# Optimization experiments

Hardware: AMD Instinct MI355X
Metric: run time of the kernel (lower is better)

## Reference

```python
import jax, jax.numpy as jnp
import numpy as np

HIDDEN = 2048
VOCAB = 50257


def setup_inputs() -> dict:
    key = jax.random.key(0)
    ks = jax.random.split(key, 9)
    s = 1.0 / np.sqrt(HIDDEN)
    return {
        "input": jax.random.randint(ks[0], (1,), 0, VOCAB, dtype=jnp.int64) if jax.config.jax_enable_x64 else jax.random.randint(ks[0], (1,), 0, VOCAB, dtype=jnp.int32),
        "hidden": jax.random.normal(ks[1], (1, 1, HIDDEN), dtype=jnp.float32),
        "embedding": jax.random.normal(ks[2], (VOCAB, HIDDEN), dtype=jnp.float32),
        "w_ih": jax.random.uniform(ks[3], (3 * HIDDEN, HIDDEN), jnp.float32, -s, s),
        "w_hh": jax.random.uniform(ks[4], (3 * HIDDEN, HIDDEN), jnp.float32, -s, s),
        "b_ih": jax.random.uniform(ks[5], (3 * HIDDEN,), jnp.float32, -s, s),
        "b_hh": jax.random.uniform(ks[6], (3 * HIDDEN,), jnp.float32, -s, s),
        "out_w": jax.random.uniform(ks[7], (VOCAB, HIDDEN), jnp.float32, -s, s),
        "out_b": jax.random.uniform(ks[8], (VOCAB,), jnp.float32, -s, s),
    }


def reference(input, hidden, embedding, w_ih, w_hh, b_ih, b_hh, out_w, out_b):
    # embedding lookup + view(1,1,-1) + relu  -> x: [H]
    x = jax.nn.relu(embedding[input[0]])
    h = hidden[0, 0]  # [H]
    # PyTorch GRU single step: gates ordered (r, z, n)
    gi = w_ih @ x + b_ih  # [3H]
    gh = w_hh @ h + b_hh  # [3H]
    i_r, i_z, i_n = jnp.split(gi, 3)
    h_r, h_z, h_n = jnp.split(gh, 3)
    r = jax.nn.sigmoid(i_r + h_r)
    z = jax.nn.sigmoid(i_z + h_z)
    n = jnp.tanh(i_n + r * h_n)
    h_new = (1.0 - z) * n + z * h  # [H]
    # output projection (nn.Linear: x @ W.T + b) + log_softmax(dim=1)
    logits = out_w @ h_new + out_b  # [V]
    logp = jax.nn.log_softmax(logits)[None, :]  # [1, V]
    return logp, h_new[None, None, :]
```

## Files before the change

kernel.cpp:

```cpp
#include <hip/hip_runtime.h>
#include <math.h>

#define H 2048
#define V 50257
#define NTHR 256
#define LB 512
#define NW (LB * 4)
#define ROWS_BASE 24
#define TAIL (V - ROWS_BASE * NW)

typedef unsigned long long u64;

#if defined(__has_builtin)
#if __has_builtin(__builtin_amdgcn_global_load_lds)
#define HAS_GLL 1
#endif
#endif
#ifndef HAS_GLL
#define HAS_GLL 0
#endif

__device__ __forceinline__ float wave_reduce_sum(float v) {
#pragma unroll
    for (int off = 32; off > 0; off >>= 1)
        v += __shfl_down(v, off, 64);
    return v;
}

__device__ __forceinline__ void online_comb(float& m, float& s, float om, float os) {
    float M = fmaxf(m, om);
    s = s * __expf(m - M) + os * __expf(om - M);
    m = M;
}

#if HAS_GLL
__device__ __forceinline__ void gl2lds16(const void* g, void* l) {
    __builtin_amdgcn_global_load_lds(
        (const __attribute__((address_space(1))) void*)g,
        (__attribute__((address_space(3))) void*)l, 16, 0, 0);
}
#endif

__global__ __launch_bounds__(384) void k_gru(
    const int* __restrict__ idx_p, const float* __restrict__ emb,
    const float* __restrict__ hid,
    const float* __restrict__ w_ih, const float* __restrict__ w_hh,
    const float* __restrict__ b_ih, const float* __restrict__ b_hh,
    float* __restrict__ hnew_ws, float* __restrict__ hnew_out,
    u64* __restrict__ partials) {
    __shared__ float xs[H];
    __shared__ float hs[H];
    __shared__ float partial[6][2];
    int tid = threadIdx.x;

    if (tid == 0 && blockIdx.x < LB) partials[blockIdx.x] = 0ull;

    long idx = (long)idx_p[0];
    const float4* embrow = (const float4*)(emb + idx * (long)H);
    for (int i = tid; i < H / 4; i += 384) {
        float4 e = embrow[i];
        e.x = fmaxf(e.x, 0.f); e.y = fmaxf(e.y, 0.f);
        e.z = fmaxf(e.z, 0.f); e.w = fmaxf(e.w, 0.f);
        ((float4*)xs)[i] = e;
        ((float4*)hs)[i] = ((const float4*)hid)[i];
    }
    __syncthreads();

    int wid = tid >> 6, lane = tid & 63;
    int gate = wid % 3;
    const float* W   = (wid < 3) ? w_ih : w_hh;
    const float* vec = (wid < 3) ? xs : hs;
    int j0 = blockIdx.x, j1 = blockIdx.x + 1024;
    const float4* r0 = (const float4*)(W + ((size_t)gate * H + j0) * (size_t)H);
    const float4* r1 = (const float4*)(W + ((size_t)gate * H + j1) * (size_t)H);

    float4 vreg[8];
#pragma unroll
    for (int it = 0; it < 8; ++it)
        vreg[it] = ((const float4*)vec)[it * 64 + lane];

    float a0 = 0.f, a1 = 0.f;
#pragma unroll
    for (int it = 0; it < 8; ++it) {
        float4 wa = r0[it * 64 + lane];
        float4 wb = r1[it * 64 + lane];
        a0 += wa.x * vreg[it].x + wa.y * vreg[it].y + wa.z * vreg[it].z + wa.w * vreg[it].w;
        a1 += wb.x * vreg[it].x + wb.y * vreg[it].y + wb.z * vreg[it].z + wb.w * vreg[it].w;
    }
    a0 = wave_reduce_sum(a0);
    a1 = wave_reduce_sum(a1);
    if (lane == 0) { partial[wid][0] = a0; partial[wid][1] = a1; }
    __syncthreads();

    if (tid < 2) {
        int j = (tid == 0) ? j0 : j1;
        float i_r = partial[0][tid] + b_ih[j];
        float i_z = partial[1][tid] + b_ih[H + j];
        float i_n = partial[2][tid] + b_ih[2 * H + j];
        float h_r = partial[3][tid] + b_hh[j];
        float h_z = partial[4][tid] + b_hh[H + j];
        float h_n = partial[5][tid] + b_hh[2 * H + j];
        float r = 1.f / (1.f + expf(-(i_r + h_r)));
        float z = 1.f / (1.f + expf(-(i_z + h_z)));
        float n = tanhf(i_n + r * h_n);
        float hv = (1.f - z) * n + z * hs[j];
        hnew_ws[j] = hv;
        hnew_out[j] = hv;
    }
}

__global__ __launch_bounds__(NTHR, 2) void k_logits_fused(
    const float* __restrict__ out_w, const float* __restrict__ out_b,
    const float* __restrict__ hnew, float* __restrict__ out,
    u64* __restrict__ partials) {
    __shared__ float hsm[H];
    __shared__ float stage[4][2][H];
    __shared__ float l_lds[4][25];
    __shared__ float pm[4], ps[4];
    __shared__ float c_s;
    const int tid = threadIdx.x, wid = tid >> 6, lane = tid & 63;
    const int gw = blockIdx.x * 4 + wid;
    const int nrows = ROWS_BASE + (gw < TAIL ? 1 : 0);

    for (int i = tid; i < H / 4; i += NTHR)
        ((float4*)hsm)[i] = ((const float4*)hnew)[i];
    float bias = 0.f;
    if (lane < nrows) {
        int r = (lane < ROWS_BASE) ? (gw + lane * NW) : (ROWS_BASE * NW + gw);
        bias = out_b[r];
    }
    asm volatile("" :: "v"(bias));
    __syncthreads();

    float4 vreg[8];
#pragma unroll
    for (int it = 0; it < 8; ++it)
        vreg[it] = ((const float4*)hsm)[it * 64 + lane];

    float* slot0 = &stage[wid][0][0];
    float* slot1 = &stage[wid][1][0];

    float m = -INFINITY, s = 0.f;

#if HAS_GLL
    auto issue_row = [&](int k) {
        int r = (k < ROWS_BASE) ? (gw + k * NW) : (ROWS_BASE * NW + gw);
        const char* gb = (const char*)(out_w + (size_t)r * H) + lane * 16;
        char* lb = (char*)((k & 1) ? slot1 : slot0);
#pragma unroll
        for (int c = 0; c < 8; ++c)
            gl2lds16(gb + c * 1024, lb + c * 1024);
    };

    issue_row(0);
    issue_row(1);
#pragma unroll 1
    for (int k = 0; k < nrows; ++k) {
        if (k == nrows - 1) {
            asm volatile("s_waitcnt vmcnt(0)" ::: "memory");
        } else {
            asm volatile("s_waitcnt vmcnt(8)" ::: "memory");
        }
        __builtin_amdgcn_sched_barrier(0);
        const float4* s4 = (const float4*)((k & 1) ? slot1 : slot0);
        float acc = 0.f;
#pragma unroll
        for (int it = 0; it < 8; ++it) {
            float4 w4 = s4[it * 64 + lane];
            acc += w4.x * vreg[it].x + w4.y * vreg[it].y + w4.z * vreg[it].z + w4.w * vreg[it].w;
        }
        acc = wave_reduce_sum(acc);
        float bk = __shfl(bias, k, 64);
        if (lane == 0) {
            float l = acc + bk;
            l_lds[wid][k] = l;
            online_comb(m, s, l, 1.0f);
        }
        if (k + 2 < nrows) issue_row(k + 2);
    }
#else
#pragma unroll 1
    for (int k = 0; k < nrows; ++k) {
        int r = (k < ROWS_BASE) ? (gw + k * NW) : (ROWS_BASE * NW + gw);
        const float4* row = (const float4*)(out_w + (size_t)r * H);
        float acc = 0.f;
#pragma unroll
        for (int it = 0; it < 8; ++it) {
            float4 w4 = row[it * 64 + lane];
            acc += w4.x * vreg[it].x + w4.y * vreg[it].y + w4.z * vreg[it].z + w4.w * vreg[it].w;
        }
        acc = wave_reduce_sum(acc);
        float bk = __shfl(bias, k, 64);
        if (lane == 0) {
            float l = acc + bk;
            l_lds[wid][k] = l;
            online_comb(m, s, l, 1.0f);
        }
    }
#endif

    if (lane == 0) { pm[wid] = m; ps[wid] = s; }
    __syncthreads();

    if (tid == 0) {
        float M = pm[0], S = ps[0];
        online_comb(M, S, pm[1], ps[1]);
        online_comb(M, S, pm[2], ps[2]);
        online_comb(M, S, pm[3], ps[3]);
        u64 pk = ((u64)__float_as_uint(S) << 32) | (u64)__float_as_uint(M);
        __hip_atomic_store(&partials[blockIdx.x], pk, __ATOMIC_RELAXED,
                           __HIP_MEMORY_SCOPE_AGENT);
    }
    __syncthreads();

    float mm = -INFINITY, ss = 0.f;
    for (int i = tid; i < LB; i += NTHR) {
        u64 pk;
        while ((pk = __hip_atomic_load(&partials[i], __ATOMIC_RELAXED,
                                       __HIP_MEMORY_SCOPE_AGENT)) == 0ull)
            __builtin_amdgcn_s_sleep(8);
        float pmv = __uint_as_float((unsigned)(pk & 0xffffffffu));
        float psv = __uint_as_float((unsigned)(pk >> 32));
        online_comb(mm, ss, pmv, psv);
    }
#pragma unroll
    for (int off = 32; off > 0; off >>= 1) {
        float om = __shfl_down(mm, off, 64);
        float os = __shfl_down(ss, off, 64);
        online_comb(mm, ss, om, os);
    }
    if (lane == 0) { pm[wid] = mm; ps[wid] = ss; }
    __syncthreads();
    if (tid == 0) {
        float M = pm[0], S = ps[0];
        online_comb(M, S, pm[1], ps[1]);
        online_comb(M, S, pm[2], ps[2]);
        online_comb(M, S, pm[3], ps[3]);
        c_s = M + logf(S);
    }
    __syncthreads();
    const float C = c_s;

    if (lane < ROWS_BASE) {
        out[gw + lane * NW] = l_lds[wid][lane] - C;
    } else if (lane == ROWS_BASE && gw < TAIL) {
        out[ROWS_BASE * NW + gw] = l_lds[wid][ROWS_BASE] - C;
    }
}

extern "C" void kernel_launch(void* const* d_in, const int* in_sizes, int n_in,
                              void* d_out, int out_size, void* d_ws, size_t ws_size,
                              hipStream_t stream) {
    const int*   idx    = (const int*)d_in[0];
    const float* hidden = (const float*)d_in[1];
    const float* emb    = (const float*)d_in[2];
    const float* w_ih   = (const float*)d_in[3];
    const float* w_hh   = (const float*)d_in[4];
    const float* b_ih   = (const float*)d_in[5];
    const float* b_hh   = (const float*)d_in[6];
    const float* out_w  = (const float*)d_in[7];
    const float* out_b  = (const float*)d_in[8];

    float* out = (float*)d_out;
    float* ws  = (float*)d_ws;
    float* hnew     = ws;
    u64*   partials = (u64*)(ws + H);

    k_gru<<<1024, 384, 0, stream>>>(idx, emb, hidden, w_ih, w_hh, b_ih, b_hh,
                                    hnew, out + V, partials);
    k_logits_fused<<<LB, NTHR, 0, stream>>>(out_w, out_b, hnew, out, partials);
}
```

Before: 97.39 us.

## Double logits grid and halve per-row staging units to raise occupancy

Doubles the number of logits blocks (LB 512→1024) so each wave handles about 12 rows instead of 24. Each row is now staged through LDS in two half-row units, and the h_new vector is loaded straight from global memory into registers, so the LDS footprint per block shrinks and launch bounds allow 4 blocks per SM. The goal is more waves in flight to hide HBM latency on the out_w stream. In exchange the pipeline is shallower (two half-rows in flight), and the partials buffer and the final combine now span more blocks.

```diff
diff --git a/kernel.cpp b/kernel.cpp
--- a/kernel.cpp
+++ b/kernel.cpp
@@ -4,9 +4,9 @@
 #define H 2048
 #define V 50257
 #define NTHR 256
-#define LB 512
+#define LB 1024
 #define NW (LB * 4)
-#define ROWS_BASE 24
+#define ROWS_BASE 12
 #define TAIL (V - ROWS_BASE * NW)
 
 typedef unsigned long long u64;
@@ -53,7 +53,7 @@
     __shared__ float partial[6][2];
     int tid = threadIdx.x;
 
-    if (tid == 0 && blockIdx.x < LB) partials[blockIdx.x] = 0ull;
+    if (tid == 0) partials[blockIdx.x] = 0ull;
 
     long idx = (long)idx_p[0];
     const float4* embrow = (const float4*)(emb + idx * (long)H);
@@ -109,74 +109,75 @@
     }
 }
 
-__global__ __launch_bounds__(NTHR, 2) void k_logits_fused(
+__global__ __launch_bounds__(NTHR, 4) void k_logits_fused(
     const float* __restrict__ out_w, const float* __restrict__ out_b,
     const float* __restrict__ hnew, float* __restrict__ out,
     u64* __restrict__ partials) {
-    __shared__ float hsm[H];
-    __shared__ float stage[4][2][H];
-    __shared__ float l_lds[4][25];
+    __shared__ float stage[4][2][1024];
+    __shared__ float l_lds[4][13];
     __shared__ float pm[4], ps[4];
     __shared__ float c_s;
     const int tid = threadIdx.x, wid = tid >> 6, lane = tid & 63;
     const int gw = blockIdx.x * 4 + wid;
     const int nrows = ROWS_BASE + (gw < TAIL ? 1 : 0);
 
-    for (int i = tid; i < H / 4; i += NTHR)
-        ((float4*)hsm)[i] = ((const float4*)hnew)[i];
+    float4 vreg[8];
+#pragma unroll
+    for (int it = 0; it < 8; ++it)
+        vreg[it] = ((const float4*)hnew)[it * 64 + lane];
     float bias = 0.f;
     if (lane < nrows) {
         int r = (lane < ROWS_BASE) ? (gw + lane * NW) : (ROWS_BASE * NW + gw);
         bias = out_b[r];
     }
-    asm volatile("" :: "v"(bias));
-    __syncthreads();
-
-    float4 vreg[8];
-#pragma unroll
-    for (int it = 0; it < 8; ++it)
-        vreg[it] = ((const float4*)hsm)[it * 64 + lane];
-
+
+    float m = -INFINITY, s = 0.f;
+
+#if HAS_GLL
     float* slot0 = &stage[wid][0][0];
     float* slot1 = &stage[wid][1][0];
-
-    float m = -INFINITY, s = 0.f;
-
-#if HAS_GLL
-    auto issue_row = [&](int k) {
+    auto issue_unit = [&](int u) {
+        int k = u >> 1, h = u & 1;
         int r = (k < ROWS_BASE) ? (gw + k * NW) : (ROWS_BASE * NW + gw);
-        const char* gb = (const char*)(out_w + (size_t)r * H) + lane * 16;
-        char* lb = (char*)((k & 1) ? slot1 : slot0);
-#pragma unroll
-        for (int c = 0; c < 8; ++c)
+        const char* gb = (const char*)(out_w + (size_t)r * H + h * 1024) + lane * 16;
+        char* lb = (char*)((u & 1) ? slot1 : slot0);
+#pragma unroll
+        for (int c = 0; c < 4; ++c)
             gl2lds16(gb + c * 1024, lb + c * 1024);
     };
 
-    issue_row(0);
-    issue_row(1);
+    const int U = 2 * nrows;
+    issue_unit(0);
+    issue_unit(1);
+    float acc = 0.f;
 #pragma unroll 1
-    for (int k = 0; k < nrows; ++k) {
-        if (k == nrows - 1) {
+    for (int u = 0; u < U; ++u) {
+        if (u == U - 1) {
             asm volatile("s_waitcnt vmcnt(0)" ::: "memory");
         } else {
-            asm volatile("s_waitcnt vmcnt(8)" ::: "memory");
+            asm volatile("s_waitcnt vmcnt(4)" ::: "memory");
         }
         __builtin_amdgcn_sched_barrier(0);
-        const float4* s4 = (const float4*)((k & 1) ? slot1 : slot0);
-        float acc = 0.f;
-#pragma unroll
-        for (int it = 0; it < 8; ++it) {
+        const float4* s4 = (const float4*)((u & 1) ? slot1 : slot0);
+        const int hb = (u & 1) * 4;
+#pragma unroll
+        for (int it = 0; it < 4; ++it) {
             float4 w4 = s4[it * 64 + lane];
-            acc += w4.x * vreg[it].x + w4.y * vreg[it].y + w4.z * vreg[it].z + w4.w * vreg[it].w;
-        }
-        acc = wave_reduce_sum(acc);
-        float bk = __shfl(bias, k, 64);
-        if (lane == 0) {
-            float l = acc + bk;
-            l_lds[wid][k] = l;
-            online_comb(m, s, l, 1.0f);
-        }
-        if (k + 2 < nrows) issue_row(k + 2);
+            acc += w4.x * vreg[hb + it].x + w4.y * vreg[hb + it].y +
+                   w4.z * vreg[hb + it].z + w4.w * vreg[hb + it].w;
+        }
+        if (u & 1) {
+            int k = u >> 1;
+            float t = wave_reduce_sum(acc);
+            float bk = __shfl(bias, k, 64);
+            if (lane == 0) {
+                float l = t + bk;
+                l_lds[wid][k] = l;
+                online_comb(m, s, l, 1.0f);
+            }
+            acc = 0.f;
+        }
+        if (u + 2 < U) issue_unit(u + 2);
     }
 #else
 #pragma unroll 1
```

After: 159.3 us. +63.6%, slower.
